# Kernel tuning notes

Measured on AMD Instinct MI355X. Metric: run time of the kernel, lower is better.

## Reference

```python
import jax, jax.numpy as jnp
import numpy as np

NU, NI = 16384, 8192          # num_users, num_items
DK, DM = 64, 64               # embed_k, embed_k_multimod
DV, DT = 4096, 384            # visual / textual feature dims
TOP_K = 10
N_LAYERS = 1                  # item-graph propagation layers
N_UI_LAYERS = 2               # user-item LGConv layers
L_M = 0.7
E = 524288                    # user-item interactions (doubled to symmetric edges)


def build_sim(x):
    # cosine similarity: row-normalize then x @ x.T  -> [N, N]
    xn = x / jnp.linalg.norm(x, axis=-1, keepdims=True)
    return xn @ xn.T


def build_knn(sim, k):
    # keep top-k values per row, zero elsewhere (torch topk + scatter_)
    vals, idx = jax.lax.top_k(sim, k)
    rows = jnp.arange(sim.shape[0])[:, None]
    return jnp.zeros_like(sim).at[rows, idx].set(vals)


def normalized_laplacian(adj):
    # D^{-1/2} A D^{-1/2}; inf (zero-degree) -> 0, applied as row/col scaling
    d = adj.sum(-1)
    dis = jnp.where(d > 0, jax.lax.rsqrt(jnp.where(d > 0, d, 1.0)), 0.0)
    return adj * dis[:, None] * dis[None, :]


def l2_normalize(x, axis=-1, eps=1e-12):
    n = jnp.linalg.norm(x, axis=axis, keepdims=True)
    return x / jnp.maximum(n, eps)


def setup_inputs() -> dict:
    key = jax.random.key(0)
    ks = jax.random.split(key, 8)
    Gu = jax.random.normal(ks[0], (NU, DK), jnp.float32) * 0.1
    Gi = jax.random.normal(ks[1], (NI, DK), jnp.float32) * 0.1
    feat_v = jax.random.normal(ks[2], (NI, DV), jnp.float32)
    feat_t = jax.random.normal(ks[3], (NI, DT), jnp.float32)
    W_v = jax.random.normal(ks[4], (DV, DM), jnp.float32) / np.sqrt(DV)
    b_v = jnp.zeros((DM,), jnp.float32)
    W_t = jax.random.normal(ks[5], (DT, DM), jnp.float32) / np.sqrt(DT)
    b_t = jnp.zeros((DM,), jnp.float32)
    importance_weights = jnp.full((2,), 0.5, jnp.float32)
    # precomputed per-modality normalized laplacians from raw (detached) features
    Sim_v = normalized_laplacian(build_knn(build_sim(feat_v), TOP_K))
    Sim_t = normalized_laplacian(build_knn(build_sim(feat_t), TOP_K))
    # symmetric bipartite user-item edge list (items offset by NU)
    u = jax.random.randint(ks[6], (E,), 0, NU)
    i = jax.random.randint(ks[7], (E,), 0, NI) + NU
    edge_index = jnp.stack([jnp.concatenate([u, i]), jnp.concatenate([i, u])])
    return dict(Gu=Gu, Gi=Gi, feat_v=feat_v, feat_t=feat_t, W_v=W_v, b_v=b_v,
                W_t=W_t, b_t=b_t, importance_weights=importance_weights,
                Sim_v=Sim_v, Sim_t=Sim_t, edge_index=edge_index)


def propagate(Gu, Gi, feat_v, feat_t, W_v, b_v, W_t, b_t,
              importance_weights, Sim_v, Sim_t, edge_index):
    w = jax.nn.softmax(importance_weights)
    learned = jnp.zeros((NI, NI), jnp.float32)
    original = jnp.zeros((NI, NI), jnp.float32)
    for m, (feat, W, b, Sim) in enumerate(
            [(feat_v, W_v, b_v, Sim_v), (feat_t, W_t, b_t, Sim_t)]):
        proj = feat @ W + b                                  # [NI, DM]
        learned = learned + w[m] * build_knn(build_sim(proj), TOP_K)
        original = original + w[m] * Sim
    Si = (1.0 - L_M) * normalized_laplacian(learned) + L_M * original
    # item-graph propagation
    item_emb = Gi
    for _ in range(N_LAYERS):
        item_emb = Si @ item_emb                              # [NI, DK]
    # user-item LGConv (normalize=False => plain sum aggregation)
    src, dst = edge_index[0], edge_index[1]
    all_emb = [jnp.concatenate([Gu, Gi], 0)]                  # [NU+NI, DK]
    for _ in range(N_UI_LAYERS):
        agg = jax.ops.segment_sum(all_emb[-1][src], dst, num_segments=NU + NI)
        all_emb.append(l2_normalize(agg, axis=1))
    mean_emb = jnp.stack(all_emb, 1).mean(1)
    gu, gi = mean_emb[:NU], mean_emb[NU:]
    return gu, gi + l2_normalize(item_emb, axis=1)


def reference(Gu, Gi, feat_v, feat_t, W_v, b_v, W_t, b_t,
              importance_weights, Sim_v, Sim_t, edge_index):
    return propagate(Gu, Gi, feat_v, feat_t, W_v, b_v, W_t, b_t,
                     importance_weights, Sim_v, Sim_t, edge_index)
```

## Files before the change

### kernel.cpp

```cpp
#include <hip/hip_runtime.h>
#include <hip/hip_bf16.h>

#define NU 16384
#define NI 8192
#define TOPK 10
#define NTOT (NU + NI)
#define OCAP 64
#define NSEG 4
#define CSEG (NI / NSEG)
#define NGRP 512
#define MAXSEL 16

typedef short short8v __attribute__((ext_vector_type(8)));
typedef float float4v __attribute__((ext_vector_type(4)));

__device__ __forceinline__ float warp64_sum(float v) {
#pragma unroll
  for (int m = 32; m >= 1; m >>= 1) v += __shfl_xor(v, m);
  return v;
}

__device__ __forceinline__ unsigned int umap(float f) {
  unsigned int b = __float_as_uint(f);
  return b ^ ((b & 0x80000000u) ? 0xFFFFFFFFu : 0x80000000u);
}

__global__ __launch_bounds__(256) void fused_proj_hist_kernel(
    const float* __restrict__ feat, const float* __restrict__ W,
    float* __restrict__ partial, int D, int kchunk,
    const int* __restrict__ dst, int* __restrict__ deg, int nedge) {
  __shared__ float sA[64][64];
  __shared__ float sB[64][68];
  const int tid = threadIdx.x;
  if (blockIdx.x >= 1024) {
    int e = (blockIdx.x - 1024) * 256 + tid;
    if (e < nedge) atomicAdd(&deg[dst[e]], 1);
    return;
  }
  const int pb = blockIdx.x;
  const int r0 = (pb & 127) * 64;
  const int ks = pb >> 7;
  const int rg = tid >> 4, cg = tid & 15;
  const int rA = tid & 63, kgA = (tid >> 6) * 16;
  const int kB = tid & 63, cbB = (tid >> 6) * 16;
  const int kbeg = ks * kchunk, kend = kbeg + kchunk;
  float4 pa[4], pb4[4];
  {
    const float* fp = feat + (size_t)(r0 + rA) * D + kbeg + kgA;
    pa[0] = *(const float4*)(fp + 0);  pa[1] = *(const float4*)(fp + 4);
    pa[2] = *(const float4*)(fp + 8);  pa[3] = *(const float4*)(fp + 12);
    const float* wp = W + (size_t)(kbeg + kB) * 64 + cbB;
    pb4[0] = *(const float4*)(wp + 0);  pb4[1] = *(const float4*)(wp + 4);
    pb4[2] = *(const float4*)(wp + 8);  pb4[3] = *(const float4*)(wp + 12);
  }
  float acc[4][4] = {{0,0,0,0},{0,0,0,0},{0,0,0,0},{0,0,0,0}};
  for (int kc = kbeg; kc < kend; kc += 64) {
#pragma unroll
    for (int i = 0; i < 4; ++i) {
      sA[kgA + 4*i + 0][rA] = pa[i].x;
      sA[kgA + 4*i + 1][rA] = pa[i].y;
      sA[kgA + 4*i + 2][rA] = pa[i].z;
      sA[kgA + 4*i + 3][rA] = pa[i].w;
      *(float4*)&sB[kB][cbB + 4*i] = pb4[i];
    }
    __syncthreads();
    if (kc + 64 < kend) {
      const float* fp = feat + (size_t)(r0 + rA) * D + kc + 64 + kgA;
      pa[0] = *(const float4*)(fp + 0);  pa[1] = *(const float4*)(fp + 4);
      pa[2] = *(const float4*)(fp + 8);  pa[3] = *(const float4*)(fp + 12);
      const float* wp = W + (size_t)(kc + 64 + kB) * 64 + cbB;
      pb4[0] = *(const float4*)(wp + 0);  pb4[1] = *(const float4*)(wp + 4);
      pb4[2] = *(const float4*)(wp + 8);  pb4[3] = *(const float4*)(wp + 12);
    }
#pragma unroll 8
    for (int k = 0; k < 64; ++k) {
      float4 a = *(const float4*)&sA[k][rg * 4];
      float4 b = *(const float4*)&sB[k][cg * 4];
      acc[0][0] += a.x * b.x; acc[0][1] += a.x * b.y; acc[0][2] += a.x * b.z; acc[0][3] += a.x * b.w;
      acc[1][0] += a.y * b.x; acc[1][1] += a.y * b.y; acc[1][2] += a.y * b.z; acc[1][3] += a.y * b.w;
      acc[2][0] += a.z * b.x; acc[2][1] += a.z * b.y; acc[2][2] += a.z * b.z; acc[2][3] += a.z * b.w;
      acc[3][0] += a.w * b.x; acc[3][1] += a.w * b.y; acc[3][2] += a.w * b.z; acc[3][3] += a.w * b.w;
    }
    __syncthreads();
  }
#pragma unroll
  for (int rr = 0; rr < 4; ++rr) {
    float4 o = make_float4(acc[rr][0], acc[rr][1], acc[rr][2], acc[rr][3]);
    *(float4*)(partial + ((size_t)ks * NI + r0 + rg * 4 + rr) * 64 + cg * 4) = o;
  }
}

__global__ __launch_bounds__(256) void proj_partial_kernel(
    const float* __restrict__ feat, const float* __restrict__ W,
    float* __restrict__ partial, int D, int kchunk) {
  __shared__ float sA[64][64];
  __shared__ float sB[64][68];
  const int tid = threadIdx.x;
  const int r0 = blockIdx.x * 64;
  const int ks = blockIdx.y;
  const int rg = tid >> 4, cg = tid & 15;
  const int rA = tid & 63, kgA = (tid >> 6) * 16;
  const int kB = tid & 63, cbB = (tid >> 6) * 16;
  const int kbeg = ks * kchunk, kend = kbeg + kchunk;
  float4 pa[4], pb[4];
  {
    const float* fp = feat + (size_t)(r0 + rA) * D + kbeg + kgA;
    pa[0] = *(const float4*)(fp + 0);  pa[1] = *(const float4*)(fp + 4);
    pa[2] = *(const float4*)(fp + 8);  pa[3] = *(const float4*)(fp + 12);
    const float* wp = W + (size_t)(kbeg + kB) * 64 + cbB;
    pb[0] = *(const float4*)(wp + 0);  pb[1] = *(const float4*)(wp + 4);
    pb[2] = *(const float4*)(wp + 8);  pb[3] = *(const float4*)(wp + 12);
  }
  float acc[4][4] = {{0,0,0,0},{0,0,0,0},{0,0,0,0},{0,0,0,0}};
  for (int kc = kbeg; kc < kend; kc += 64) {
#pragma unroll
    for (int i = 0; i < 4; ++i) {
      sA[kgA + 4*i + 0][rA] = pa[i].x;
      sA[kgA + 4*i + 1][rA] = pa[i].y;
      sA[kgA + 4*i + 2][rA] = pa[i].z;
      sA[kgA + 4*i + 3][rA] = pa[i].w;
      *(float4*)&sB[kB][cbB + 4*i] = pb[i];
    }
    __syncthreads();
    if (kc + 64 < kend) {
      const float* fp = feat + (size_t)(r0 + rA) * D + kc + 64 + kgA;
      pa[0] = *(const float4*)(fp + 0);  pa[1] = *(const float4*)(fp + 4);
      pa[2] = *(const float4*)(fp + 8);  pa[3] = *(const float4*)(fp + 12);
      const float* wp = W + (size_t)(kc + 64 + kB) * 64 + cbB;
      pb[0] = *(const float4*)(wp + 0);  pb[1] = *(const float4*)(wp + 4);
      pb[2] = *(const float4*)(wp + 8);  pb[3] = *(const float4*)(wp + 12);
    }
#pragma unroll 8
    for (int k = 0; k < 64; ++k) {
      float4 a = *(const float4*)&sA[k][rg * 4];
      float4 b = *(const float4*)&sB[k][cg * 4];
      acc[0][0] += a.x * b.x; acc[0][1] += a.x * b.y; acc[0][2] += a.x * b.z; acc[0][3] += a.x * b.w;
      acc[1][0] += a.y * b.x; acc[1][1] += a.y * b.y; acc[1][2] += a.y * b.z; acc[1][3] += a.y * b.w;
      acc[2][0] += a.z * b.x; acc[2][1] += a.z * b.y; acc[2][2] += a.z * b.z; acc[2][3] += a.z * b.w;
      acc[3][0] += a.w * b.x; acc[3][1] += a.w * b.y; acc[3][2] += a.w * b.z; acc[3][3] += a.w * b.w;
    }
    __syncthreads();
  }
#pragma unroll
  for (int rr = 0; rr < 4; ++rr) {
    float4 o = make_float4(acc[rr][0], acc[rr][1], acc[rr][2], acc[rr][3]);
    *(float4*)(partial + ((size_t)ks * NI + r0 + rg * 4 + rr) * 64 + cg * 4) = o;
  }
}

__global__ __launch_bounds__(256) void proj_reduce_kernel(
    const float* __restrict__ partial, const float* __restrict__ b, int ksplit,
    float* __restrict__ xn, ushort* __restrict__ hi, ushort* __restrict__ lo) {
  const int row = blockIdx.x * 4 + (threadIdx.x >> 6);
  const int col = threadIdx.x & 63;
  float acc = b[col];
  for (int ks = 0; ks < ksplit; ++ks)
    acc += partial[((size_t)ks * NI + row) * 64 + col];
  float ss = warp64_sum(acc * acc);
  float v = acc * (1.0f / sqrtf(ss));
  xn[(size_t)row * 64 + col] = v;
  __hip_bfloat16 hb = __float2bfloat16(v);
  float hf = __bfloat162float(hb);
  __hip_bfloat16 lb = __float2bfloat16(v - hf);
  hi[(size_t)row * 64 + col] = *(ushort*)&hb;
  lo[(size_t)row * 64 + col] = *(ushort*)&lb;
}

__global__ __launch_bounds__(256) void fused_sim_kernel(
    const float* __restrict__ Sv, const float* __restrict__ St,
    const float* __restrict__ iw, int* __restrict__ ocols,
    float* __restrict__ ow, int* __restrict__ ocnt,
    const ushort* __restrict__ hiV, const ushort* __restrict__ loV,
    const ushort* __restrict__ hiT, const ushort* __restrict__ loT,
    float* __restrict__ tmax) {
  __shared__ ushort sH[64][64];
  __shared__ ushort sL[64][64];
  const int tid = threadIdx.x;
  const int bid = blockIdx.x;
  if (bid >= 1024) {
    const int lane = tid & 63;
    const int row = (bid - 1024) * 4 + (tid >> 6);
    float ea = expf(iw[0]), eb = expf(iw[1]);
    float wA = 0.7f * ea / (ea + eb), wB = 0.7f * eb / (ea + eb);
    int cnt = 0;
    int* oc = ocols + (size_t)row * OCAP;
    float* op = ow + (size_t)row * OCAP;
#pragma unroll 1
    for (int m = 0; m < 2; ++m) {
      const float* S = m ? St : Sv;
      float wgt = m ? wB : wA;
      const float4* rp = (const float4*)(S + (size_t)row * NI);
      float4 cur = rp[lane];
#pragma unroll 1
      for (int it = 0; it < NI / 256; ++it) {
        float4 nxt;
        if (it + 1 < NI / 256) nxt = rp[(it + 1) * 64 + lane];
        bool anynz = (cur.x != 0.0f) | (cur.y != 0.0f) | (cur.z != 0.0f) | (cur.w != 0.0f);
        if (__ballot(anynz) != 0ull) {
          int cb = it * 256 + lane * 4;
#pragma unroll
          for (int j = 0; j < 4; ++j) {
            float x = (j == 0) ? cur.x : (j == 1) ? cur.y : (j == 2) ? cur.z : cur.w;
            bool nz = (x != 0.0f);
            unsigned long long mk = __ballot(nz);
            int pre = __popcll(mk & ((1ull << lane) - 1ull));
            if (nz) {
              int p = cnt + pre;
              if (p < OCAP) { oc[p] = cb + j; op[p] = wgt * x; }
            }
            cnt += __popcll(mk);
          }
        }
        cur = nxt;
      }
    }
    if (lane == 0) ocnt[row] = (cnt < OCAP) ? cnt : OCAP;
    return;
  }
  const int t2 = bid;
  const int m = t2 >> 9;
  const int rest = t2 & 511;
  const int seg = rest >> 7;
  const int r_base = (rest & 127) * 64;
  const ushort* hi = m ? hiT : hiV;
  const ushort* lo = m ? loT : loV;
  const int c_base = seg * CSEG;
  const int wave = tid >> 6, lane = tid & 63;
  const int lr = lane & 15, lg = lane >> 4;
  const int my_row = r_base + wave * 16 + lr;
  short8v bh[2], bl[2];
  {
    const ushort* rp = hi + (size_t)my_row * 64 + lg * 8;
    bh[0] = *(const short8v*)(rp);
    bh[1] = *(const short8v*)(rp + 32);
    const ushort* rp2 = lo + (size_t)my_row * 64 + lg * 8;
    bl[0] = *(const short8v*)(rp2);
    bl[1] = *(const short8v*)(rp2 + 32);
  }
  float* tbase = tmax + ((size_t)m * NI + my_row) * NGRP + seg * (CSEG / 16);
  const int sc = tid >> 2, sq = (tid & 3) * 32;
  const int sw = (sc & 7) << 4;
  for (int c0 = 0; c0 < CSEG; c0 += 64) {
    __syncthreads();
    const char* gh = (const char*)(hi + (size_t)(c_base + c0 + sc) * 64);
    const char* gl2 = (const char*)(lo + (size_t)(c_base + c0 + sc) * 64);
    *(float4*)((char*)&sH[sc][0] + (sq ^ sw)) = *(const float4*)(gh + sq);
    *(float4*)((char*)&sH[sc][0] + ((sq + 16) ^ sw)) = *(const float4*)(gh + sq + 16);
    *(float4*)((char*)&sL[sc][0] + (sq ^ sw)) = *(const float4*)(gl2 + sq);
    *(float4*)((char*)&sL[sc][0] + ((sq + 16) ^ sw)) = *(const float4*)(gl2 + sq + 16);
    __syncthreads();
#pragma unroll
    for (int s = 0; s < 4; ++s) {
      const int ca = s * 16 + lr;
      const int cw = (ca & 7) << 4;
      const int kb0 = (lg * 16) ^ cw;
      const int kb1 = (lg * 16 + 64) ^ cw;
      short8v ah0 = *(const short8v*)((const char*)&sH[ca][0] + kb0);
      short8v ah1 = *(const short8v*)((const char*)&sH[ca][0] + kb1);
      short8v al0 = *(const short8v*)((const char*)&sL[ca][0] + kb0);
      short8v al1 = *(const short8v*)((const char*)&sL[ca][0] + kb1);
      float4v acc = {0.f, 0.f, 0.f, 0.f};
      acc = __builtin_amdgcn_mfma_f32_16x16x32_bf16(ah0, bh[0], acc, 0, 0, 0);
      acc = __builtin_amdgcn_mfma_f32_16x16x32_bf16(ah1, bh[1], acc, 0, 0, 0);
      acc = __builtin_amdgcn_mfma_f32_16x16x32_bf16(ah0, bl[0], acc, 0, 0, 0);
      acc = __builtin_amdgcn_mfma_f32_16x16x32_bf16(ah1, bl[1], acc, 0, 0, 0);
      acc = __builtin_amdgcn_mfma_f32_16x16x32_bf16(al0, bh[0], acc, 0, 0, 0);
      acc = __builtin_amdgcn_mfma_f32_16x16x32_bf16(al1, bh[1], acc, 0, 0, 0);
      float gm = fmaxf(fmaxf(acc[0], acc[1]), fmaxf(acc[2], acc[3]));
      gm = fmaxf(gm, __shfl_xor(gm, 16));
      gm = fmaxf(gm, __shfl_xor(gm, 32));
      if (lg == 0) tbase[(c0 >> 4) + s] = gm;
    }
  }
}

__global__ __launch_bounds__(256) void fused_rescore_fill_kernel(
    const float* __restrict__ xn_v, const float* __restrict__ xn_t,
    const float* __restrict__ tmax,
    float* __restrict__ tkvV, int* __restrict__ tkiV,
    float* __restrict__ tkvT, int* __restrict__ tkiT,
    const int* __restrict__ esrc, const int* __restrict__ edst,
    int* __restrict__ cursor, int* __restrict__ csr, int nedge) {
  const int tid = threadIdx.x;
  if (blockIdx.x >= 2 * NI) {
    int e = (blockIdx.x - 2 * NI) * 256 + tid;
    if (e < nedge) {
      int p = atomicAdd(&cursor[edst[e]], 1);
      csr[p] = esrc[e];
    }
    return;
  }
  const int bid = blockIdx.x;
  const int m = bid >> 13;
  const int row = bid & (NI - 1);
  const float* xn = m ? xn_t : xn_v;
  __shared__ int ssel[MAXSEL];
  __shared__ float sval[MAXSEL * 16];
  __shared__ int scol[MAXSEL * 16];
  __shared__ float lv[32];
  __shared__ int lc[32];
  __shared__ int lnum;
  const int grp = tid >> 4, l16 = tid & 15;
  float4 rq = ((const float4*)(xn + (size_t)row * 64))[l16];
  if (tid < 64) {
    const int lane = tid;
    const float4* tmr4 = (const float4*)(tmax + ((size_t)m * NI + row) * NGRP);
    float4 t0 = tmr4[lane];
    float4 t1 = tmr4[64 + lane];
    unsigned int uv[8] = {umap(t0.x), umap(t0.y), umap(t0.z), umap(t0.w),
                          umap(t1.x), umap(t1.y), umap(t1.z), umap(t1.w)};
    unsigned long long blo = 0, bhi = 0x100000000ull;
    unsigned int taub = 0;
    for (int it = 0; it < 34; ++it) {
      unsigned int mid = (unsigned int)((blo + bhi) >> 1);
      int cnt = 0;
#pragma unroll
      for (int j = 0; j < 8; ++j) cnt += __popcll(__ballot(uv[j] >= mid));
      if (cnt >= 12) {
        taub = mid;
        if (cnt <= MAXSEL) break;
        blo = (unsigned long long)mid + 1;
      } else {
        bhi = mid;
      }
      if (blo >= bhi) break;
    }
    unsigned long long bj[8];
    int base[8];
    int tot = 0;
#pragma unroll
    for (int j = 0; j < 8; ++j) {
      bj[j] = __ballot(uv[j] >= taub);
      base[j] = tot;
      tot += __popcll(bj[j]);
    }
    if (lane < MAXSEL) ssel[lane] = -1;
    unsigned long long ltm = (1ull << lane) - 1ull;
#pragma unroll
    for (int j = 0; j < 8; ++j) {
      if (uv[j] >= taub) {
        int pos = base[j] + __popcll(bj[j] & ltm);
        if (pos < MAXSEL) {
          int g = (j < 4) ? (lane * 4 + j) : (256 + lane * 4 + (j - 4));
          ssel[pos] = g;
        }
      }
    }
  }
  __syncthreads();
  for (int it = 0; it < MAXSEL; ++it) {
    int gsel = ssel[it];
    bool valid = (gsel >= 0);
    int c = valid ? (gsel * 16 + grp) : 0;
    float4 x4 = ((const float4*)(xn + (size_t)c * 64))[l16];
    float s = rq.x * x4.x + rq.y * x4.y + rq.z * x4.z + rq.w * x4.w;
    s += __shfl_xor(s, 1);
    s += __shfl_xor(s, 2);
    s += __shfl_xor(s, 4);
    s += __shfl_xor(s, 8);
    if (l16 == 0) {
      sval[it * 16 + grp] = valid ? s : -3.0e38f;
      scol[it * 16 + grp] = valid ? c : 0x7fffffff;
    }
  }
  __syncthreads();
  if (tid < 64) {
    const int lane = tid;
    float fv[4];
    int fc[4];
    unsigned int uv4[4];
#pragma unroll
    for (int k = 0; k < 4; ++k) {
      fv[k] = sval[lane + 64 * k];
      fc[k] = scol[lane + 64 * k];
      uv4[k] = umap(fv[k]);
    }
    unsigned long long blo = 0, bhi = 0x100000000ull;
    unsigned int taub = 0;
    for (int it = 0; it < 34; ++it) {
      unsigned int mid = (unsigned int)((blo + bhi) >> 1);
      int cnt = 0;
#pragma unroll
      for (int k = 0; k < 4; ++k) cnt += __popcll(__ballot(uv4[k] >= mid));
      if (cnt >= TOPK) {
        taub = mid;
        if (cnt == TOPK) break;
        blo = (unsigned long long)mid + 1;
      } else {
        bhi = mid;
      }
      if (blo >= bhi) break;
    }
    unsigned long long bk[4];
    int base[4];
    int tot = 0;
#pragma unroll
    for (int k = 0; k < 4; ++k) {
      bk[k] = __ballot(uv4[k] >= taub);
      base[k] = tot;
      tot += __popcll(bk[k]);
    }
    float* tv = m ? tkvT : tkvV;
    int* ti = m ? tkiT : tkiV;
    unsigned long long ltm = (1ull << lane) - 1ull;
    if (tot == TOPK) {
#pragma unroll
      for (int k = 0; k < 4; ++k) {
        if (uv4[k] >= taub) {
          int pos = base[k] + __popcll(bk[k] & ltm);
          tv[(size_t)row * TOPK + pos] = fv[k];
          ti[(size_t)row * TOPK + pos] = fc[k];
        }
      }
    } else {
#pragma unroll
      for (int k = 0; k < 4; ++k) {
        if (uv4[k] >= taub) {
          int pos = base[k] + __popcll(bk[k] & ltm);
          if (pos < 32) { lv[pos] = fv[k]; lc[pos] = fc[k]; }
        }
      }
      if (lane == 0) lnum = (tot < 32) ? tot : 32;
      if (lane == 0) {
        int n = lnum;
        unsigned int used = 0;
        for (int q = 0; q < TOPK; ++q) {
          float bv = -3.0e38f;
          int bc = 0x7fffffff, bi = -1;
          for (int i2 = 0; i2 < n; ++i2) {
            if (used & (1u << i2)) continue;
            if (lv[i2] > bv || (lv[i2] == bv && lc[i2] < bc)) {
              bv = lv[i2]; bc = lc[i2]; bi = i2;
            }
          }
          used |= (1u << bi);
          tv[(size_t)row * TOPK + q] = bv;
          ti[(size_t)row * TOPK + q] = bc;
        }
      }
    }
  }
}

__global__ void dis_kernel(const float* __restrict__ tkv_v, const float* __restrict__ tkv_t,
                           const float* __restrict__ iw, float* __restrict__ dis) {
  int r = blockIdx.x * blockDim.x + threadIdx.x;
  if (r >= NI) return;
  float ea = expf(iw[0]), eb = expf(iw[1]);
  float w0 = ea / (ea + eb), w1 = eb / (ea + eb);
  float s0 = 0.f, s1 = 0.f;
  for (int j = 0; j < TOPK; ++j) { s0 += tkv_v[r * TOPK + j]; s1 += tkv_t[r * TOPK + j]; }
  float d = w0 * s0 + w1 * s1;
  dis[r] = (d > 0.0f) ? (1.0f / sqrtf(d)) : 0.0f;
}

__global__ __launch_bounds__(256) void item_emb_kernel(
    const float* __restrict__ Gi,
    const float* __restrict__ tkv_v, const int* __restrict__ tki_v,
    const float* __restrict__ tkv_t, const int* __restrict__ tki_t,
    const float* __restrict__ dis, const int* __restrict__ ocols,
    const float* __restrict__ ow, const int* __restrict__ ocnt,
    const float* __restrict__ iw, float* __restrict__ nitem) {
  const int d = threadIdx.x & 63;
  const int row = blockIdx.x * 4 + (threadIdx.x >> 6);
  float ea = expf(iw[0]), eb = expf(iw[1]);
  float w0 = ea / (ea + eb), w1 = eb / (ea + eb);
  float disr = dis[row];
  float acc = 0.0f;
#pragma unroll 1
  for (int m = 0; m < 2; ++m) {
    const float* tv = m ? tkv_t : tkv_v;
    const int* ti = m ? tki_t : tki_v;
    float wm = (m ? w1 : w0) * 0.3f * disr;
    for (int j = 0; j < TOPK; ++j) {
      float val = tv[(size_t)row * TOPK + j];
      int c = ti[(size_t)row * TOPK + j];
      acc += wm * val * dis[c] * Gi[(size_t)c * 64 + d];
    }
  }
  int cn = ocnt[row];
  for (int j = 0; j < cn; ++j) {
    int c = ocols[(size_t)row * OCAP + j];
    float wv = ow[(size_t)row * OCAP + j];
    acc += wv * Gi[(size_t)c * 64 + d];
  }
  float ss = warp64_sum(acc * acc);
  float nr = sqrtf(ss);
  nitem[(size_t)row * 64 + d] = acc / fmaxf(nr, 1e-12f);
}

__global__ __launch_bounds__(256) void scanA_kernel(
    const int* __restrict__ deg, int* __restrict__ loc, int* __restrict__ bsum) {
  __shared__ int s[256];
  int tid = threadIdx.x, gid = blockIdx.x * 256 + tid;
  int x = deg[gid];
  s[tid] = x;
  __syncthreads();
  for (int off = 1; off < 256; off <<= 1) {
    int t = (tid >= off) ? s[tid - off] : 0;
    __syncthreads();
    s[tid] += t;
    __syncthreads();
  }
  loc[gid] = s[tid] - x;
  if (tid == 255) bsum[blockIdx.x] = s[255];
}

__global__ __launch_bounds__(256) void scanC_kernel(
    const int* __restrict__ loc, const int* __restrict__ bsum,
    int* __restrict__ row_ptr, int* __restrict__ cursor, int n) {
  int gid = blockIdx.x * blockDim.x + threadIdx.x;
  if (gid > n) return;
  int blk = gid >> 8;
  int off = 0;
  for (int b2 = 0; b2 < blk; ++b2) off += bsum[b2];
  if (gid == n) { row_ptr[n] = off; return; }
  int v = off + loc[gid];
  row_ptr[gid] = v;
  cursor[gid] = v;
}

__global__ __launch_bounds__(256) void segsum_kernel(
    const float* __restrict__ inU, const float* __restrict__ inI,
    const int* __restrict__ row_ptr, const int* __restrict__ csr,
    float* __restrict__ outp) {
  const int d = threadIdx.x & 63;
  const int row = blockIdx.x * 4 + (threadIdx.x >> 6);
  int a = row_ptr[row], bnd = row_ptr[row + 1];
  float acc = 0.0f;
  for (int e = a; e < bnd; ++e) {
    int s = csr[e];
    const float* sp = (s < NU) ? (inU + (size_t)s * 64) : (inI + (size_t)(s - NU) * 64);
    acc += sp[d];
  }
  float ss = warp64_sum(acc * acc);
  float nr = sqrtf(ss);
  outp[(size_t)row * 64 + d] = acc / fmaxf(nr, 1e-12f);
}

__global__ __launch_bounds__(256) void segsum_final_kernel(
    const float* __restrict__ e1b, const int* __restrict__ row_ptr,
    const int* __restrict__ csr, const float* __restrict__ Gu,
    const float* __restrict__ Gi, const float* __restrict__ nitem,
    float* __restrict__ outp) {
  const int d = threadIdx.x & 63;
  const int row = blockIdx.x * 4 + (threadIdx.x >> 6);
  const float* inU = e1b;
  const float* inI = e1b + (size_t)NU * 64;
  int a = row_ptr[row], bnd = row_ptr[row + 1];
  float acc = 0.0f;
  for (int e = a; e < bnd; ++e) {
    int s = csr[e];
    const float* sp = (s < NU) ? (inU + (size_t)s * 64) : (inI + (size_t)(s - NU) * 64);
    acc += sp[d];
  }
  float ss = warp64_sum(acc * acc);
  float e2 = acc / fmaxf(sqrtf(ss), 1e-12f);
  float base = (row < NU) ? Gu[(size_t)row * 64 + d] : Gi[(size_t)(row - NU) * 64 + d];
  float v = (base + e1b[(size_t)row * 64 + d] + e2) * (1.0f / 3.0f);
  if (row >= NU) v += nitem[(size_t)(row - NU) * 64 + d];
  outp[(size_t)row * 64 + d] = v;
}

extern "C" void kernel_launch(void* const* d_in, const int* in_sizes, int n_in,
                              void* d_out, int out_size, void* d_ws, size_t ws_size,
                              hipStream_t stream) {
  const float* Gu = (const float*)d_in[0];
  const float* Gi = (const float*)d_in[1];
  const float* feat_v = (const float*)d_in[2];
  const float* feat_t = (const float*)d_in[3];
  const float* W_v = (const float*)d_in[4];
  const float* b_v = (const float*)d_in[5];
  const float* W_t = (const float*)d_in[6];
  const float* b_t = (const float*)d_in[7];
  const float* iw = (const float*)d_in[8];
  const float* Sv = (const float*)d_in[9];
  const float* St = (const float*)d_in[10];
  const int* eidx = (const int*)d_in[11];
  const int twoE = in_sizes[11] / 2;
  const int* esrc = eidx;
  const int* edst = eidx + twoE;
  float* outp = (float*)d_out;

  char* w = (char*)d_ws;
  size_t off = 0;
  auto alloc = [&](size_t bytes) -> void* {
    void* p = w + off;
    off = (off + bytes + 255) & ~(size_t)255;
    return p;
  };
  float* xn_v = (float*)alloc((size_t)NI * 64 * 4);
  float* xn_t = (float*)alloc((size_t)NI * 64 * 4);
  ushort* hiV = (ushort*)alloc((size_t)NI * 64 * 2);
  ushort* loV = (ushort*)alloc((size_t)NI * 64 * 2);
  ushort* hiT = (ushort*)alloc((size_t)NI * 64 * 2);
  ushort* loT = (ushort*)alloc((size_t)NI * 64 * 2);
  float* tmax = (float*)alloc((size_t)2 * NI * NGRP * 4);
  float* tkvV = (float*)alloc((size_t)NI * TOPK * 4);
  int* tkiV = (int*)alloc((size_t)NI * TOPK * 4);
  float* tkvT = (float*)alloc((size_t)NI * TOPK * 4);
  int* tkiT = (int*)alloc((size_t)NI * TOPK * 4);
  float* dis = (float*)alloc((size_t)NI * 4);
  int* ocols = (int*)alloc((size_t)NI * OCAP * 4);
  float* ow = (float*)alloc((size_t)NI * OCAP * 4);
  int* ocnt = (int*)alloc((size_t)NI * 4);
  float* nitem = (float*)alloc((size_t)NI * 64 * 4);
  float* e1b = (float*)alloc((size_t)NTOT * 64 * 4);
  int* deg = (int*)alloc((size_t)NTOT * 4);
  int* row_ptr = (int*)alloc((size_t)(NTOT + 1) * 4);
  int* cursor = (int*)alloc((size_t)NTOT * 4);
  int* csr = (int*)alloc((size_t)twoE * 4);
  int* locb = (int*)alloc((size_t)NTOT * 4);
  int* bsum = (int*)alloc((size_t)(NTOT / 256) * 4);
  if (off > ws_size) return;

  float* partial = tmax;

  hipMemsetAsync(deg, 0, (size_t)NTOT * 4, stream);

  fused_proj_hist_kernel<<<1024 + 4096, 256, 0, stream>>>(
      feat_v, W_v, partial, 4096, 512, edst, deg, twoE);
  proj_reduce_kernel<<<NI / 4, 256, 0, stream>>>(partial, b_v, 8, xn_v, hiV, loV);
  proj_partial_kernel<<<dim3(NI / 64, 6), 256, 0, stream>>>(feat_t, W_t, partial, 384, 64);
  proj_reduce_kernel<<<NI / 4, 256, 0, stream>>>(partial, b_t, 6, xn_t, hiT, loT);
  scanA_kernel<<<NTOT / 256, 256, 0, stream>>>(deg, locb, bsum);
  scanC_kernel<<<(NTOT + 1 + 255) / 256, 256, 0, stream>>>(locb, bsum, row_ptr, cursor, NTOT);
  fused_sim_kernel<<<1024 + 2048, 256, 0, stream>>>(
      Sv, St, iw, ocols, ow, ocnt, hiV, loV, hiT, loT, tmax);
  fused_rescore_fill_kernel<<<2 * NI + 4096, 256, 0, stream>>>(
      xn_v, xn_t, tmax, tkvV, tkiV, tkvT, tkiT, esrc, edst, cursor, csr, twoE);
  dis_kernel<<<(NI + 255) / 256, 256, 0, stream>>>(tkvV, tkvT, iw, dis);
  item_emb_kernel<<<NI / 4, 256, 0, stream>>>(Gi, tkvV, tkiV, tkvT, tkiT, dis, ocols, ow,
                                              ocnt, iw, nitem);
  segsum_kernel<<<NTOT / 4, 256, 0, stream>>>(Gu, Gi, row_ptr, csr, e1b);
  segsum_final_kernel<<<NTOT / 4, 256, 0, stream>>>(e1b, row_ptr, csr, Gu, Gi, nitem, outp);
}
```

Measured before the change: 659.8 us.

## Shift CSR fill and segsum earlier, fuse item embedding into final pass

Moves the CSR fill blocks into the similarity kernel, runs the first segsum layer as extra blocks inside the rescore kernel, and folds the item-graph propagation into the final segsum kernel. Two launches and the nitem intermediate buffer go away, and independent work now shares launches to fill idle compute units. The catch is that item rows in the final kernel carry extra gather work, which makes the load uneven across waves.

```diff
diff --git a/kernel.cpp b/kernel.cpp
--- a/kernel.cpp
+++ b/kernel.cpp
@@ -172,12 +172,14 @@
     float* __restrict__ ow, int* __restrict__ ocnt,
     const ushort* __restrict__ hiV, const ushort* __restrict__ loV,
     const ushort* __restrict__ hiT, const ushort* __restrict__ loT,
-    float* __restrict__ tmax) {
+    float* __restrict__ tmax,
+    const int* __restrict__ esrc, const int* __restrict__ edst,
+    int* __restrict__ cursor, int* __restrict__ csr, int nedge) {
   __shared__ ushort sH[64][64];
   __shared__ ushort sL[64][64];
   const int tid = threadIdx.x;
   const int bid = blockIdx.x;
-  if (bid >= 1024) {
+  if (bid >= 1024 && bid < 3072) {
     const int lane = tid & 63;
     const int row = (bid - 1024) * 4 + (tid >> 6);
     float ea = expf(iw[0]), eb = expf(iw[1]);
@@ -217,6 +219,14 @@
     if (lane == 0) ocnt[row] = (cnt < OCAP) ? cnt : OCAP;
     return;
   }
+  if (bid >= 3072) {
+    int e = (bid - 3072) * 256 + tid;
+    if (e < nedge) {
+      int p = atomicAdd(&cursor[edst[e]], 1);
+      csr[p] = esrc[e];
+    }
+    return;
+  }
   const int t2 = bid;
   const int m = t2 >> 9;
   const int rest = t2 & 511;
@@ -274,20 +284,28 @@
   }
 }
 
-__global__ __launch_bounds__(256) void fused_rescore_fill_kernel(
+__global__ __launch_bounds__(256) void fused_rescore_segsum_kernel(
     const float* __restrict__ xn_v, const float* __restrict__ xn_t,
     const float* __restrict__ tmax,
     float* __restrict__ tkvV, int* __restrict__ tkiV,
     float* __restrict__ tkvT, int* __restrict__ tkiT,
-    const int* __restrict__ esrc, const int* __restrict__ edst,
-    int* __restrict__ cursor, int* __restrict__ csr, int nedge) {
+    const float* __restrict__ Gu, const float* __restrict__ Gi,
+    const int* __restrict__ row_ptr, const int* __restrict__ csr,
+    float* __restrict__ e1b) {
   const int tid = threadIdx.x;
   if (blockIdx.x >= 2 * NI) {
-    int e = (blockIdx.x - 2 * NI) * 256 + tid;
-    if (e < nedge) {
-      int p = atomicAdd(&cursor[edst[e]], 1);
-      csr[p] = esrc[e];
-    }
+    const int d = tid & 63;
+    const int row = (blockIdx.x - 2 * NI) * 4 + (tid >> 6);
+    int a = row_ptr[row], bnd = row_ptr[row + 1];
+    float acc = 0.0f;
+    for (int e = a; e < bnd; ++e) {
+      int s = csr[e];
+      const float* sp = (s < NU) ? (Gu + (size_t)s * 64) : (Gi + (size_t)(s - NU) * 64);
+      acc += sp[d];
+    }
+    float ss = warp64_sum(acc * acc);
+    float nr = sqrtf(ss);
+    e1b[(size_t)row * 64 + d] = acc / fmaxf(nr, 1e-12f);
     return;
   }
   const int bid = blockIdx.x;
@@ -454,41 +472,6 @@
   dis[r] = (d > 0.0f) ? (1.0f / sqrtf(d)) : 0.0f;
 }
 
-__global__ __launch_bounds__(256) void item_emb_kernel(
-    const float* __restrict__ Gi,
-    const float* __restrict__ tkv_v, const int* __restrict__ tki_v,
-    const float* __restrict__ tkv_t, const int* __restrict__ tki_t,
-    const float* __restrict__ dis, const int* __restrict__ ocols,
-    const float* __restrict__ ow, const int* __restrict__ ocnt,
-    const float* __restrict__ iw, float* __restrict__ nitem) {
-  const int d = threadIdx.x & 63;
-  const int row = blockIdx.x * 4 + (threadIdx.x >> 6);
-  float ea = expf(iw[0]), eb = expf(iw[1]);
-  float w0 = ea / (ea + eb), w1 = eb / (ea + eb);
-  float disr = dis[row];
-  float acc = 0.0f;
-#pragma unroll 1
-  for (int m = 0; m < 2; ++m) {
-    const float* tv = m ? tkv_t : tkv_v;
-    const int* ti = m ? tki_t : tki_v;
-    float wm = (m ? w1 : w0) * 0.3f * disr;
-    for (int j = 0; j < TOPK; ++j) {
-      float val = tv[(size_t)row * TOPK + j];
-      int c = ti[(size_t)row * TOPK + j];
-      acc += wm * val * dis[c] * Gi[(size_t)c * 64 + d];
-    }
-  }
-  int cn = ocnt[row];
-  for (int j = 0; j < cn; ++j) {
-    int c = ocols[(size_t)row * OCAP + j];
-    float wv = ow[(size_t)row * OCAP + j];
-    acc += wv * Gi[(size_t)c * 64 + d];
-  }
-  float ss = warp64_sum(acc * acc);
-  float nr = sqrtf(ss);
-  nitem[(size_t)row * 64 + d] = acc / fmaxf(nr, 1e-12f);
-}
-
 __global__ __launch_bounds__(256) void scanA_kernel(
     const int* __restrict__ deg, int* __restrict__ loc, int* __restrict__ bsum) {
   __shared__ int s[256];
@@ -520,29 +503,15 @@
   cursor[gid] = v;
 }
 
-__global__ __launch_bounds__(256) void segsum_kernel(
-    const float* __restrict__ inU, const float* __restrict__ inI,
-    const int* __restrict__ row_ptr, const int* __restrict__ csr,
-    float* __restrict__ outp) {
-  const int d = threadIdx.x & 63;
-  const int row = blockIdx.x * 4 + (threadIdx.x >> 6);
-  int a = row_ptr[row], bnd = row_ptr[row + 1];
-  float acc = 0.0f;
-  for (int e = a; e < bnd; ++e) {
-    int s = csr[e];
-    const float* sp = (s < NU) ? (inU + (size_t)s * 64) : (inI + (size_t)(s - NU) * 64);
-    acc += sp[d];
-  }
-  float ss = warp64_sum(acc * acc);
-  float nr = sqrtf(ss);
-  outp[(size_t)row * 64 + d] = acc / fmaxf(nr, 1e-12f);
-}
-
 __global__ __launch_bounds__(256) void segsum_final_kernel(
     const float* __restrict__ e1b, const int* __restrict__ row_ptr,
     const int* __restrict__ csr, const float* __restrict__ Gu,
-    const float* __restrict__ Gi, const float* __restrict__ nitem,
-    float* __restrict__ outp) {
+    const float* __restrict__ Gi,
+    const float* __restrict__ tkv_v, const int* __restrict__ tki_v,
+    const float* __restrict__ tkv_t, const int* __restrict__ tki_t,
+    const float* __restrict__ dis, const int* __restrict__ ocols,
+    const float* __restrict__ ow, const int* __restrict__ ocnt,
+    const float* __restrict__ iw, float* __restrict__ outp) {
   const int d = threadIdx.x & 63;
   const int row = blockIdx.x * 4 + (threadIdx.x >> 6);
   const float* inU = e1b;
@@ -558,7 +527,32 @@
   float e2 = acc / fmaxf(sqrtf(ss), 1e-12f);
   float base = (row < NU) ? Gu[(size_t)row * 64 + d] : Gi[(size_t)(row - NU) * 64 + d];
   float v = (base + e1b[(size_t)row * 64 + d] + e2) * (1.0f / 3.0f);
-  if (row >= NU) v += nitem[(size_t)(row - NU) * 64 + d];
+  if (row >= NU) {
+    const int ir = row - NU;
+    float ea = expf(iw[0]), eb = expf(iw[1]);
+    float w0 = ea / (ea + eb), w1 = eb / (ea + eb);
+    float disr = dis[ir];
+    float iacc = 0.0f;
+#pragma unroll 1
+    for (int m = 0; m < 2; ++m) {
+      const float* tv = m ? tkv_t : tkv_v;
+      const int* ti = m ? tki_t : tki_v;
+      float wm = (m ? w1 : w0) * 0.3f * disr;
+      for (int j = 0; j < TOPK; ++j) {
+        float val = tv[(size_t)ir * TOPK + j];
+        int c = ti[(size_t)ir * TOPK + j];
+        iacc += wm * val * dis[c] * Gi[(size_t)c * 64 + d];
+      }
+    }
+    int cn = ocnt[ir];
+    for (int j = 0; j < cn; ++j) {
+      int c = ocols[(size_t)ir * OCAP + j];
+      float wv = ow[(size_t)ir * OCAP + j];
+      iacc += wv * Gi[(size_t)c * 64 + d];
+    }
+    float iss = warp64_sum(iacc * iacc);
+    v += iacc / fmaxf(sqrtf(iss), 1e-12f);
+  }
   outp[(size_t)row * 64 + d] = v;
 }
 
@@ -604,7 +598,6 @@
   int* ocols = (int*)alloc((size_t)NI * OCAP * 4);
   float* ow = (float*)alloc((size_t)NI * OCAP * 4);
   int* ocnt = (int*)alloc((size_t)NI * 4);
-  float* nitem = (float*)alloc((size_t)NI * 64 * 4);
   float* e1b = (float*)alloc((size_t)NTOT * 64 * 4);
   int* deg = (int*)alloc((size_t)NTOT * 4);
   int* row_ptr = (int*)alloc((size_t)(NTOT + 1) * 4);
@@ -625,13 +618,13 @@
   proj_reduce_kernel<<<NI / 4, 256, 0, stream>>>(partial, b_t, 6, xn_t, hiT, loT);
   scanA_kernel<<<NTOT / 256, 256, 0, stream>>>(deg, locb, bsum);
   scanC_kernel<<<(NTOT + 1 + 255) / 256, 256, 0, stream>>>(locb, bsum, row_ptr, cursor, NTOT);
-  fused_sim_kernel<<<1024 + 2048, 256, 0, stream>>>(
-      Sv, St, iw, ocols, ow, ocnt, hiV, loV, hiT, loT, tmax);
-  fused_rescore_fill_kernel<<<2 * NI + 4096, 256, 0, stream>>>(
-      xn_v, xn_t, tmax, tkvV, tkiV, tkvT, tkiT, esrc, edst, cursor, csr, twoE);
+  fused_sim_kernel<<<1024 + 2048 + 4096, 256, 0, stream>>>(
+      Sv, St, iw, ocols, ow, ocnt, hiV, loV, hiT, loT, tmax,
+      esrc, edst, cursor, csr, twoE);
+  fused_rescore_segsum_kernel<<<2 * NI + NTOT / 4, 256, 0, stream>>>(
+      xn_v, xn_t, tmax, tkvV, tkiV, tkvT, tkiT, Gu, Gi, row_ptr, csr, e1b);
   dis_kernel<<<(NI + 255) / 256, 256, 0, stream>>>(tkvV, tkvT, iw, dis);
-  item_emb_kernel<<<NI / 4, 256, 0, stream>>>(Gi, tkvV, tkiV, tkvT, tkiT, dis, ocols, ow,
-                                              ocnt, iw, nitem);
-  segsum_kernel<<<NTOT / 4, 256, 0, stream>>>(Gu, Gi, row_ptr, csr, e1b);
-  segsum_final_kernel<<<NTOT / 4, 256, 0, stream>>>(e1b, row_ptr, csr, Gu, Gi, nitem, outp);
-}
+  segsum_final_kernel<<<NTOT / 4, 256, 0, stream>>>(
+      e1b, row_ptr, csr, Gu, Gi, tkvV, tkiV, tkvT, tkiT, dis, ocols, ow, ocnt,
+      iw, outp);
+}
```

New measurement: 670.6 us. Within noise of the previous version (+1.7%).
